# Kernel tuning notes

Hardware: AMD Instinct MI355X
Metric: run time of the kernel (lower is better)

Reference implementation:

```python
import jax, jax.numpy as jnp
import numpy as np

INPUT_DIM = 512
HIDDEN_DIM = 1024


def glorot_normal(key, shape):
    fan_in, fan_out = shape[0], shape[1]
    std = jnp.sqrt(2.0 / (fan_in + fan_out))
    return std * jax.random.normal(key, shape, dtype=jnp.float32)


def setup_inputs() -> dict:
    key = jax.random.key(0)
    k1, k2, k3 = jax.random.split(key, 3)
    b, t = 32, 1024
    H = HIDDEN_DIM + INPUT_DIM
    x_btd = jax.random.normal(k1, (b, t, INPUT_DIM), dtype=jnp.float32)
    input_paddings = jnp.zeros((b, t), dtype=jnp.float32)
    kernel = glorot_normal(k2, (H, 4 * HIDDEN_DIM))  # [H, 4h]
    bias = jnp.zeros((4 * HIDDEN_DIM,), dtype=jnp.float32)
    h_init = glorot_normal(k3, (1, HIDDEN_DIM))
    return {"x_btd": x_btd, "input_paddings": input_paddings,
            "kernel": kernel, "bias": bias, "h_init": h_init}


def lstm_step(carry, x_bd, kernel, bias):
    h_bh, c_bh = carry
    x_bH = jnp.concatenate([x_bd, h_bh], axis=-1)          # [b, d+h]
    gate_out = jnp.einsum('bH,Hh->bh', x_bH, kernel) + bias  # [b, 4h]
    f, i, o, g = jnp.split(gate_out, 4, axis=-1)
    c_new = jax.nn.sigmoid(f) * c_bh + jax.nn.sigmoid(i) * jnp.tanh(g)
    h_new = jax.nn.sigmoid(o) * jnp.tanh(c_new)
    return (h_new, c_new), h_new


def reference(x_btd, input_paddings, kernel, bias, h_init) -> jnp.ndarray:
    del input_paddings
    b = x_btd.shape[0]
    h0 = jnp.tile(h_init, (b, 1))                # [b, h]
    c0 = jnp.zeros((b, HIDDEN_DIM), dtype=x_btd.dtype)
    x_tbd = jnp.transpose(x_btd, (1, 0, 2))      # [t, b, d]

    def step(carry, x_bd):
        return lstm_step(carry, x_bd, kernel, bias)

    _, h_tbh = jax.lax.scan(step, (h0, c0), x_tbd)
    return jnp.transpose(h_tbh, (1, 0, 2))       # [b, t, h]
```

## Files before the change

### kernel.cpp

```cpp
#include <hip/hip_runtime.h>


#define T_STEPS 1024
#define BATCH   32
#define DIN     512
#define HID     1024
#define KTOT    1536
#define NBLK    128
#define WCOLS   32
#define WSTR    1544
#define REDSTR  33
#define REDW    (32*REDSTR)
#define NSLOT   8
#define FLAGSTR 16

#define LDS_W_BYTES   (WCOLS*WSTR*2)
#define LDS_RED_BYTES (NSLOT*REDW*4)
#define LDS_H_BYTES   (256*2)
#define LDS_TOTAL     (LDS_W_BYTES + LDS_RED_BYTES + LDS_H_BYTES)

typedef __attribute__((ext_vector_type(8))) short  short8;
typedef __attribute__((ext_vector_type(4))) float  floatx4;
typedef __attribute__((ext_vector_type(4))) unsigned short ushort4_;

__device__ __forceinline__ unsigned short f2bf(float f) {
    unsigned u = __builtin_bit_cast(unsigned, f);
    u += 0x7FFFu + ((u >> 16) & 1u);
    return (unsigned short)(u >> 16);
}
__device__ __forceinline__ float sigf(float x) { return 1.f / (1.f + __expf(-x)); }
__device__ __forceinline__ float tanh_fast(float x) {
    float e = __expf(2.f * x);
    return 1.f - 2.f / (e + 1.f);
}

__device__ __forceinline__ floatx4 coh_load16(const void* p) {
    floatx4 v;
    asm volatile("global_load_dwordx4 %0, %1, off sc1" : "=v"(v) : "v"(p));
    return v;
}
__device__ __forceinline__ int coh_load4(const void* p) {
    int v;
    asm volatile("global_load_dword %0, %1, off sc1\n\ts_waitcnt vmcnt(0)"
                 : "=v"(v) : "v"(p) : "memory");
    return v;
}
__device__ __forceinline__ void coh_store16(void* p, short8 v) {
    asm volatile("global_store_dwordx4 %0, %1, off sc1" :: "v"(p), "v"(v) : "memory");
}
__device__ __forceinline__ void coh_store4(void* p, int v) {
    asm volatile("global_store_dword %0, %1, off sc1" :: "v"(p), "v"(v) : "memory");
}
__device__ __forceinline__ void wait_vm0() {
    asm volatile("s_waitcnt vmcnt(0)" ::: "memory");
}

__global__ __launch_bounds__(256) void prep_wt(const float* __restrict__ kern,
                                               unsigned short* __restrict__ wt) {
    __shared__ unsigned short tile[64][72];
    const int c0 = (blockIdx.x & 63) * 64;
    const int k0 = (blockIdx.x >> 6) * 64;
    const int cl = threadIdx.x & 63;
    const int kg = threadIdx.x >> 6;
    #pragma unroll
    for (int i = 0; i < 16; ++i) {
        int kl = kg * 16 + i;
        tile[cl][kl] = f2bf(kern[(k0 + kl) * 4096 + c0 + cl]);
    }
    __syncthreads();
    #pragma unroll
    for (int i = 0; i < 16; ++i) {
        int cc = kg * 16 + i;
        wt[(size_t)(c0 + cc) * KTOT + k0 + cl] = tile[cc][cl];
    }
}

__global__ __launch_bounds__(256) void prep_x(const float* __restrict__ x,
                                              unsigned short* __restrict__ xT) {
    const int row = blockIdx.x * 2 + (threadIdx.x >> 7);
    const int l   = threadIdx.x & 127;
    const int b = row >> 10, t = row & 1023;
    float4 v = ((const float4*)(x + (size_t)row * DIN))[l];
    ushort4_ o;
    o.x = f2bf(v.x); o.y = f2bf(v.y); o.z = f2bf(v.z); o.w = f2bf(v.w);
    *(ushort4_*)(xT + ((size_t)t * BATCH + b) * DIN + l * 4) = o;
}

__global__ __launch_bounds__(256) void init_h(const float* __restrict__ h_init,
                                              unsigned short* __restrict__ hbuf,
                                              int* __restrict__ flags) {
    if (blockIdx.x == 32) {
        for (int i = threadIdx.x; i < NBLK * FLAGSTR; i += 256) flags[i] = 0;
        return;
    }
    const int p0 = blockIdx.x * 4;
    const int u = threadIdx.x & 7;
    #pragma unroll
    for (int j = 0; j < 4; ++j) {
        const int p = p0 + j;
        hbuf[p * 256 + threadIdx.x] = f2bf(h_init[p * 8 + u]);
    }
}

__global__ __launch_bounds__(512, 2) void lstm_persist(
    const unsigned short* __restrict__ wt,
    const unsigned short* __restrict__ xT,
    unsigned short* __restrict__ hbuf,
    int* __restrict__ flags,
    const float* __restrict__ bias,
    float* __restrict__ out)
{
    extern __shared__ char smem[];
    unsigned short* ldsW = (unsigned short*)smem;
    float* red = (float*)(smem + LDS_W_BYTES);
    unsigned short* hLDS = (unsigned short*)(smem + LDS_W_BYTES + LDS_RED_BYTES);

    const int bk   = blockIdx.x;
    const int tid  = threadIdx.x;
    const int wave = tid >> 6;
    const int lane = tid & 63;
    const int lrow = lane & 15;
    const int kq   = lane >> 4;
    const bool isG = wave < 4;
    const int  sl  = wave & 3;

    for (int cl = wave; cl < WCOLS; cl += 8) {
        const int gcol = (cl >> 3) * HID + bk * 8 + (cl & 7);
        const unsigned short* src = wt + (size_t)gcol * KTOT;
        unsigned short* dst = ldsW + cl * WSTR;
        for (int k = lane * 8; k < KTOT; k += 512)
            *(short8*)(dst + k) = *(const short8*)(src + k);
    }

    const int pb = tid >> 3;
    const int pu = tid & 7;
    float bias_r[4];
    float c_state = 0.f;
    if (tid < 256) {
        #pragma unroll
        for (int g = 0; g < 4; ++g) bias_r[g] = bias[g * HID + bk * 8 + pu];
    }

    const int* myflag = flags + (sl * 32 + (lane & 31)) * FLAGSTR;
    __syncthreads();

    {
        floatx4 zero = {0.f, 0.f, 0.f, 0.f};
        floatx4 acc[2][2];
        acc[0][0] = zero; acc[0][1] = zero; acc[1][0] = zero; acc[1][1] = zero;
        if (isG) {
            const unsigned short* xb = xT;
            #pragma unroll
            for (int i = 0; i < 4; ++i) {
                const int kl = sl * 128 + i * 32 + kq * 8;
                short8 a0 = *(const short8*)(xb + lrow * DIN + kl);
                short8 a1 = *(const short8*)(xb + (lrow + 16) * DIN + kl);
                short8 b0 = *(const short8*)(ldsW + lrow * WSTR + kl);
                short8 b1 = *(const short8*)(ldsW + (lrow + 16) * WSTR + kl);
                acc[0][0] = __builtin_amdgcn_mfma_f32_16x16x32_bf16(a0, b0, acc[0][0], 0, 0, 0);
                acc[0][1] = __builtin_amdgcn_mfma_f32_16x16x32_bf16(a0, b1, acc[0][1], 0, 0, 0);
                acc[1][0] = __builtin_amdgcn_mfma_f32_16x16x32_bf16(a1, b0, acc[1][0], 0, 0, 0);
                acc[1][1] = __builtin_amdgcn_mfma_f32_16x16x32_bf16(a1, b1, acc[1][1], 0, 0, 0);
            }
        } else {
            floatx4 ha[8][2];
            #pragma unroll
            for (int i = 0; i < 8; ++i) {
                const int p = sl * 32 + i * 4 + kq;
                ha[i][0] = coh_load16(hbuf + p * 256 + lrow * 8);
                ha[i][1] = coh_load16(hbuf + p * 256 + (lrow + 16) * 8);
            }
            wait_vm0();
            __builtin_amdgcn_sched_barrier(0);
            #pragma unroll
            for (int i = 0; i < 8; ++i) {
                const int kw = 512 + sl * 256 + i * 32 + kq * 8;
                short8 a0 = __builtin_bit_cast(short8, ha[i][0]);
                short8 a1 = __builtin_bit_cast(short8, ha[i][1]);
                short8 b0 = *(const short8*)(ldsW + lrow * WSTR + kw);
                short8 b1 = *(const short8*)(ldsW + (lrow + 16) * WSTR + kw);
                acc[0][0] = __builtin_amdgcn_mfma_f32_16x16x32_bf16(a0, b0, acc[0][0], 0, 0, 0);
                acc[0][1] = __builtin_amdgcn_mfma_f32_16x16x32_bf16(a0, b1, acc[0][1], 0, 0, 0);
                acc[1][0] = __builtin_amdgcn_mfma_f32_16x16x32_bf16(a1, b0, acc[1][0], 0, 0, 0);
                acc[1][1] = __builtin_amdgcn_mfma_f32_16x16x32_bf16(a1, b1, acc[1][1], 0, 0, 0);
            }
        }
        #pragma unroll
        for (int mt = 0; mt < 2; ++mt)
            #pragma unroll
            for (int nt = 0; nt < 2; ++nt)
                #pragma unroll
                for (int r = 0; r < 4; ++r)
                    red[wave * REDW + (mt * 16 + kq * 4 + r) * REDSTR + (nt * 16 + lrow)]
                        = acc[mt][nt][r];
    }

    for (int t = 0; t < T_STEPS; ++t) {
        __syncthreads();

        floatx4 xa[4][2];
        if (isG && t + 1 < T_STEPS) {
            const unsigned short* xb = xT + (size_t)(t + 1) * (BATCH * DIN);
            #pragma unroll
            for (int i = 0; i < 4; ++i) {
                const int kl = sl * 128 + i * 32 + kq * 8;
                xa[i][0] = *(const floatx4*)(xb + lrow * DIN + kl);
                xa[i][1] = *(const floatx4*)(xb + (lrow + 16) * DIN + kl);
            }
        }

        float gv[4];
        if (tid < 256) {
            #pragma unroll
            for (int g = 0; g < 4; ++g) {
                const int col = g * 8 + pu;
                float s = bias_r[g];
                #pragma unroll
                for (int w = 0; w < NSLOT; ++w) s += red[w * REDW + pb * REDSTR + col];
                gv[g] = s;
            }
            const float fg = sigf(gv[0]);
            const float ig = sigf(gv[1]);
            const float og = sigf(gv[2]);
            const float gg = tanh_fast(gv[3]);
            c_state = fg * c_state + ig * gg;
            const float hn = og * tanh_fast(c_state);
            out[(size_t)pb * (T_STEPS * HID) + (size_t)t * HID + bk * 8 + pu] = hn;
            hLDS[tid] = f2bf(hn);
        }
        if (t == T_STEPS - 1) break;

        __syncthreads();

        floatx4 zero = {0.f, 0.f, 0.f, 0.f};
        floatx4 acc[2][2];
        acc[0][0] = zero; acc[0][1] = zero; acc[1][0] = zero; acc[1][1] = zero;

        if (isG) {
            if (wave == 0) {
                if (lane < 32) {
                    short8 v = *(const short8*)(hLDS + lane * 8);
                    unsigned short* hp = hbuf + (size_t)((t + 1) & 1) * (NBLK * 256)
                                              + bk * 256 + lane * 8;
                    coh_store16(hp, v);
                }
                wait_vm0();
                if (lane == 0)
                    coh_store4(flags + bk * FLAGSTR, t + 1);
            }
            #pragma unroll
            for (int i = 0; i < 4; ++i) {
                const int kl = sl * 128 + i * 32 + kq * 8;
                short8 a0 = __builtin_bit_cast(short8, xa[i][0]);
                short8 a1 = __builtin_bit_cast(short8, xa[i][1]);
                short8 b0 = *(const short8*)(ldsW + lrow * WSTR + kl);
                short8 b1 = *(const short8*)(ldsW + (lrow + 16) * WSTR + kl);
                acc[0][0] = __builtin_amdgcn_mfma_f32_16x16x32_bf16(a0, b0, acc[0][0], 0, 0, 0);
                acc[0][1] = __builtin_amdgcn_mfma_f32_16x16x32_bf16(a0, b1, acc[0][1], 0, 0, 0);
                acc[1][0] = __builtin_amdgcn_mfma_f32_16x16x32_bf16(a1, b0, acc[1][0], 0, 0, 0);
                acc[1][1] = __builtin_amdgcn_mfma_f32_16x16x32_bf16(a1, b1, acc[1][1], 0, 0, 0);
            }
        } else {
            const int tgt = t + 1;
            while (coh_load4(myflag) < tgt)
                __builtin_amdgcn_s_sleep(1);
            const unsigned short* hb = hbuf + (size_t)((t + 1) & 1) * (NBLK * 256);
            floatx4 ha[8][2];
            #pragma unroll
            for (int i = 0; i < 8; ++i) {
                const int p = sl * 32 + i * 4 + kq;
                ha[i][0] = coh_load16(hb + p * 256 + lrow * 8);
                ha[i][1] = coh_load16(hb + p * 256 + (lrow + 16) * 8);
            }
            wait_vm0();
            __builtin_amdgcn_sched_barrier(0);
            #pragma unroll
            for (int i = 0; i < 8; ++i) {
                const int kw = 512 + sl * 256 + i * 32 + kq * 8;
                short8 a0 = __builtin_bit_cast(short8, ha[i][0]);
                short8 a1 = __builtin_bit_cast(short8, ha[i][1]);
                short8 b0 = *(const short8*)(ldsW + lrow * WSTR + kw);
                short8 b1 = *(const short8*)(ldsW + (lrow + 16) * WSTR + kw);
                acc[0][0] = __builtin_amdgcn_mfma_f32_16x16x32_bf16(a0, b0, acc[0][0], 0, 0, 0);
                acc[0][1] = __builtin_amdgcn_mfma_f32_16x16x32_bf16(a0, b1, acc[0][1], 0, 0, 0);
                acc[1][0] = __builtin_amdgcn_mfma_f32_16x16x32_bf16(a1, b0, acc[1][0], 0, 0, 0);
                acc[1][1] = __builtin_amdgcn_mfma_f32_16x16x32_bf16(a1, b1, acc[1][1], 0, 0, 0);
            }
        }

        #pragma unroll
        for (int mt = 0; mt < 2; ++mt)
            #pragma unroll
            for (int nt = 0; nt < 2; ++nt)
                #pragma unroll
                for (int r = 0; r < 4; ++r)
                    red[wave * REDW + (mt * 16 + kq * 4 + r) * REDSTR + (nt * 16 + lrow)]
                        = acc[mt][nt][r];
    }
}

extern "C" void kernel_launch(void* const* d_in, const int* in_sizes, int n_in,
                              void* d_out, int out_size, void* d_ws, size_t ws_size,
                              hipStream_t stream) {
    (void)in_sizes; (void)n_in; (void)out_size;
    const float* x      = (const float*)d_in[0];
    const float* kern   = (const float*)d_in[2];
    const float* bias   = (const float*)d_in[3];
    const float* h_init = (const float*)d_in[4];
    float* out = (float*)d_out;

    char* ws = (char*)d_ws;
    unsigned short* wt    = (unsigned short*)(ws);
    unsigned short* xT    = (unsigned short*)(ws + 12582912);
    unsigned short* hbuf  = (unsigned short*)(ws + 12582912 + 33554432);
    int*            flags = (int*)(ws + 12582912 + 33554432 + 131072);
    (void)ws_size;

    hipFuncSetAttribute((const void*)lstm_persist,
                        hipFuncAttributeMaxDynamicSharedMemorySize, LDS_TOTAL);

    prep_wt<<<dim3(64 * 24), dim3(256), 0, stream>>>(kern, wt);
    prep_x<<<dim3(BATCH * T_STEPS / 2), dim3(256), 0, stream>>>(x, xT);
    init_h<<<dim3(33), dim3(256), 0, stream>>>(h_init, hbuf, flags);

    void* args[] = { &wt, &xT, &hbuf, &flags, &bias, &out };
    hipLaunchCooperativeKernel((const void*)lstm_persist, dim3(NBLK), dim3(512),
                               args, LDS_TOTAL, stream);
}
```

Measured before the change: 4.356 ms.

## Keep weights in registers, double-buffer LDS atomic reduction, drop per-step barrier

Each wave now holds its slice of the bf16 weight matrix in VGPRs instead of staging all weights in LDS, which removes the LDS B-operand reads inside the MFMA loops. Partial gate sums are combined with LDS float atomic adds into a double-buffered reduction array that is pre-seeded with bias, and a single wave computes the gate nonlinearities for four outputs per lane at raised priority. That wave publishes h and its flag directly, which removes the second __syncthreads per timestep. The x prefetch now happens after the current step's MFMAs. The cost is much higher register pressure from the weight fragments, and LDS atomic contention across the eight waves.

```diff
diff --git a/kernel.cpp b/kernel.cpp
--- a/kernel.cpp
+++ b/kernel.cpp
@@ -7,21 +7,16 @@
 #define HID     1024
 #define KTOT    1536
 #define NBLK    128
-#define WCOLS   32
-#define WSTR    1544
 #define REDSTR  33
-#define REDW    (32*REDSTR)
-#define NSLOT   8
+#define REDCELLS (32*REDSTR)
 #define FLAGSTR 16
-
-#define LDS_W_BYTES   (WCOLS*WSTR*2)
-#define LDS_RED_BYTES (NSLOT*REDW*4)
-#define LDS_H_BYTES   (256*2)
-#define LDS_TOTAL     (LDS_W_BYTES + LDS_RED_BYTES + LDS_H_BYTES)
 
 typedef __attribute__((ext_vector_type(8))) short  short8;
 typedef __attribute__((ext_vector_type(4))) float  floatx4;
 typedef __attribute__((ext_vector_type(4))) unsigned short ushort4_;
+typedef __attribute__((ext_vector_type(2))) unsigned int   uint2_;
+
+#define MFMA16(a,b,c) __builtin_amdgcn_mfma_f32_16x16x32_bf16(a, b, c, 0, 0, 0)
 
 __device__ __forceinline__ unsigned short f2bf(float f) {
     unsigned u = __builtin_bit_cast(unsigned, f);
@@ -32,6 +27,9 @@
 __device__ __forceinline__ float tanh_fast(float x) {
     float e = __expf(2.f * x);
     return 1.f - 2.f / (e + 1.f);
+}
+__device__ __forceinline__ void lds_add(float* p, float v) {
+    __hip_atomic_fetch_add(p, v, __ATOMIC_RELAXED, __HIP_MEMORY_SCOPE_WORKGROUP);
 }
 
 __device__ __forceinline__ floatx4 coh_load16(const void* p) {
@@ -45,8 +43,8 @@
                  : "=v"(v) : "v"(p) : "memory");
     return v;
 }
-__device__ __forceinline__ void coh_store16(void* p, short8 v) {
-    asm volatile("global_store_dwordx4 %0, %1, off sc1" :: "v"(p), "v"(v) : "memory");
+__device__ __forceinline__ void coh_store8(void* p, uint2_ v) {
+    asm volatile("global_store_dwordx2 %0, %1, off sc1" :: "v"(p), "v"(v) : "memory");
 }
 __device__ __forceinline__ void coh_store4(void* p, int v) {
     asm volatile("global_store_dword %0, %1, off sc1" :: "v"(p), "v"(v) : "memory");
@@ -110,10 +108,7 @@
     const float* __restrict__ bias,
     float* __restrict__ out)
 {
-    extern __shared__ char smem[];
-    unsigned short* ldsW = (unsigned short*)smem;
-    float* red = (float*)(smem + LDS_W_BYTES);
-    unsigned short* hLDS = (unsigned short*)(smem + LDS_W_BYTES + LDS_RED_BYTES);
+    __shared__ float red[2][REDCELLS];
 
     const int bk   = blockIdx.x;
     const int tid  = threadIdx.x;
@@ -124,43 +119,65 @@
     const bool isG = wave < 4;
     const int  sl  = wave & 3;
 
-    for (int cl = wave; cl < WCOLS; cl += 8) {
-        const int gcol = (cl >> 3) * HID + bk * 8 + (cl & 7);
-        const unsigned short* src = wt + (size_t)gcol * KTOT;
-        unsigned short* dst = ldsW + cl * WSTR;
-        for (int k = lane * 8; k < KTOT; k += 512)
-            *(short8*)(dst + k) = *(const short8*)(src + k);
-    }
-
-    const int pb = tid >> 3;
-    const int pu = tid & 7;
-    float bias_r[4];
-    float c_state = 0.f;
-    if (tid < 256) {
-        #pragma unroll
-        for (int g = 0; g < 4; ++g) bias_r[g] = bias[g * HID + bk * 8 + pu];
-    }
-
+    short8 wb[8][2];
+    if (isG) {
+        #pragma unroll
+        for (int i = 0; i < 4; ++i) {
+            const int k = sl * 128 + i * 32 + kq * 8;
+            #pragma unroll
+            for (int c = 0; c < 2; ++c) {
+                const int cl = lrow + c * 16;
+                const int gcol = (cl >> 3) * HID + bk * 8 + (cl & 7);
+                wb[i][c] = *(const short8*)(wt + (size_t)gcol * KTOT + k);
+            }
+        }
+    } else {
+        #pragma unroll
+        for (int i = 0; i < 8; ++i) {
+            const int k = 512 + sl * 256 + i * 32 + kq * 8;
+            #pragma unroll
+            for (int c = 0; c < 2; ++c) {
+                const int cl = lrow + c * 16;
+                const int gcol = (cl >> 3) * HID + bk * 8 + (cl & 7);
+                wb[i][c] = *(const short8*)(wt + (size_t)gcol * KTOT + k);
+            }
+        }
+    }
+
+    const int pb = lane & 31;
+    const int ju = (lane >> 5) * 4;
+    float bias_r[4][4];
+    float c_st[4] = {0.f, 0.f, 0.f, 0.f};
+    if (wave == 0) {
+        #pragma unroll
+        for (int g = 0; g < 4; ++g)
+            #pragma unroll
+            for (int j = 0; j < 4; ++j)
+                bias_r[g][j] = bias[g * HID + bk * 8 + ju + j];
+    }
+
+    for (int idx = tid; idx < 2 * 1024; idx += 512) {
+        const int bsel = idx >> 10, cell = idx & 1023;
+        const int row = cell >> 5, col = cell & 31;
+        red[bsel][row * REDSTR + col] = bias[(col >> 3) * HID + bk * 8 + (col & 7)];
+    }
     const int* myflag = flags + (sl * 32 + (lane & 31)) * FLAGSTR;
     __syncthreads();
 
     {
-        floatx4 zero = {0.f, 0.f, 0.f, 0.f};
-        floatx4 acc[2][2];
-        acc[0][0] = zero; acc[0][1] = zero; acc[1][0] = zero; acc[1][1] = zero;
+        const floatx4 zero = {0.f, 0.f, 0.f, 0.f};
+        floatx4 acc[2][2] = {{zero, zero}, {zero, zero}};
         if (isG) {
             const unsigned short* xb = xT;
             #pragma unroll
             for (int i = 0; i < 4; ++i) {
-                const int kl = sl * 128 + i * 32 + kq * 8;
-                short8 a0 = *(const short8*)(xb + lrow * DIN + kl);
-                short8 a1 = *(const short8*)(xb + (lrow + 16) * DIN + kl);
-                short8 b0 = *(const short8*)(ldsW + lrow * WSTR + kl);
-                short8 b1 = *(const short8*)(ldsW + (lrow + 16) * WSTR + kl);
-                acc[0][0] = __builtin_amdgcn_mfma_f32_16x16x32_bf16(a0, b0, acc[0][0], 0, 0, 0);
-                acc[0][1] = __builtin_amdgcn_mfma_f32_16x16x32_bf16(a0, b1, acc[0][1], 0, 0, 0);
-                acc[1][0] = __builtin_amdgcn_mfma_f32_16x16x32_bf16(a1, b0, acc[1][0], 0, 0, 0);
-                acc[1][1] = __builtin_amdgcn_mfma_f32_16x16x32_bf16(a1, b1, acc[1][1], 0, 0, 0);
+                const int k = sl * 128 + i * 32 + kq * 8;
+                short8 a0 = *(const short8*)(xb + lrow * DIN + k);
+                short8 a1 = *(const short8*)(xb + (lrow + 16) * DIN + k);
+                acc[0][0] = MFMA16(a0, wb[i][0], acc[0][0]);
+                acc[0][1] = MFMA16(a0, wb[i][1], acc[0][1]);
+                acc[1][0] = MFMA16(a1, wb[i][0], acc[1][0]);
+                acc[1][1] = MFMA16(a1, wb[i][1], acc[1][1]);
             }
         } else {
             floatx4 ha[8][2];
@@ -174,15 +191,12 @@
             __builtin_amdgcn_sched_barrier(0);
             #pragma unroll
             for (int i = 0; i < 8; ++i) {
-                const int kw = 512 + sl * 256 + i * 32 + kq * 8;
                 short8 a0 = __builtin_bit_cast(short8, ha[i][0]);
                 short8 a1 = __builtin_bit_cast(short8, ha[i][1]);
-                short8 b0 = *(const short8*)(ldsW + lrow * WSTR + kw);
-                short8 b1 = *(const short8*)(ldsW + (lrow + 16) * WSTR + kw);
-                acc[0][0] = __builtin_amdgcn_mfma_f32_16x16x32_bf16(a0, b0, acc[0][0], 0, 0, 0);
-                acc[0][1] = __builtin_amdgcn_mfma_f32_16x16x32_bf16(a0, b1, acc[0][1], 0, 0, 0);
-                acc[1][0] = __builtin_amdgcn_mfma_f32_16x16x32_bf16(a1, b0, acc[1][0], 0, 0, 0);
-                acc[1][1] = __builtin_amdgcn_mfma_f32_16x16x32_bf16(a1, b1, acc[1][1], 0, 0, 0);
+                acc[0][0] = MFMA16(a0, wb[i][0], acc[0][0]);
+                acc[0][1] = MFMA16(a0, wb[i][1], acc[0][1]);
+                acc[1][0] = MFMA16(a1, wb[i][0], acc[1][0]);
+                acc[1][1] = MFMA16(a1, wb[i][1], acc[1][1]);
             }
         }
         #pragma unroll
@@ -191,74 +205,94 @@
             for (int nt = 0; nt < 2; ++nt)
                 #pragma unroll
                 for (int r = 0; r < 4; ++r)
-                    red[wave * REDW + (mt * 16 + kq * 4 + r) * REDSTR + (nt * 16 + lrow)]
-                        = acc[mt][nt][r];
+                    lds_add(&red[0][(mt * 16 + kq * 4 + r) * REDSTR + nt * 16 + lrow],
+                            acc[mt][nt][r]);
+    }
+
+    floatx4 xa[4][2];
+    if (isG) {
+        const unsigned short* xb = xT + (size_t)1 * (BATCH * DIN);
+        #pragma unroll
+        for (int i = 0; i < 4; ++i) {
+            const int k = sl * 128 + i * 32 + kq * 8;
+            xa[i][0] = *(const floatx4*)(xb + lrow * DIN + k);
+            xa[i][1] = *(const floatx4*)(xb + (lrow + 16) * DIN + k);
+        }
     }
 
     for (int t = 0; t < T_STEPS; ++t) {
         __syncthreads();
-
-        floatx4 xa[4][2];
-        if (isG && t + 1 < T_STEPS) {
-            const unsigned short* xb = xT + (size_t)(t + 1) * (BATCH * DIN);
+        float* rc = &red[t & 1][0];
+        float* rn = &red[(t + 1) & 1][0];
+
+        if (wave == 0) {
+            __builtin_amdgcn_s_setprio(1);
+            float rv[4][4];
+            #pragma unroll
+            for (int g = 0; g < 4; ++g)
+                #pragma unroll
+                for (int j = 0; j < 4; ++j)
+                    rv[g][j] = rc[pb * REDSTR + g * 8 + ju + j];
+            float hn[4];
+            #pragma unroll
+            for (int j = 0; j < 4; ++j) {
+                const float fg = sigf(rv[0][j]);
+                const float ig = sigf(rv[1][j]);
+                const float og = sigf(rv[2][j]);
+                const float gg = tanh_fast(rv[3][j]);
+                c_st[j] = fg * c_st[j] + ig * gg;
+                hn[j] = og * tanh_fast(c_st[j]);
+            }
+            if (t + 1 < T_STEPS) {
+                uint2_ hv;
+                hv.x = (unsigned)f2bf(hn[0]) | ((unsigned)f2bf(hn[1]) << 16);
+                hv.y = (unsigned)f2bf(hn[2]) | ((unsigned)f2bf(hn[3]) << 16);
+                coh_store8(hbuf + (size_t)((t + 1) & 1) * (NBLK * 256)
+                                + bk * 256 + pb * 8 + (lane >> 5) * 4, hv);
+                wait_vm0();
+                if (lane == 0) coh_store4(flags + bk * FLAGSTR, t + 1);
+            }
+            __builtin_amdgcn_s_setprio(0);
+            #pragma unroll
+            for (int g = 0; g < 4; ++g)
+                #pragma unroll
+                for (int j = 0; j < 4; ++j)
+                    rc[pb * REDSTR + g * 8 + ju + j] = bias_r[g][j];
+            floatx4 ov = {hn[0], hn[1], hn[2], hn[3]};
+            *(floatx4*)(out + (size_t)pb * (T_STEPS * HID) + (size_t)t * HID
+                        + bk * 8 + ju) = ov;
+        }
+
+        if (t + 1 >= T_STEPS) break;
+
+        const floatx4 zero = {0.f, 0.f, 0.f, 0.f};
+        floatx4 acc[2][2] = {{zero, zero}, {zero, zero}};
+        if (isG) {
             #pragma unroll
             for (int i = 0; i < 4; ++i) {
-                const int kl = sl * 128 + i * 32 + kq * 8;
-                xa[i][0] = *(const floatx4*)(xb + lrow * DIN + kl);
-                xa[i][1] = *(const floatx4*)(xb + (lrow + 16) * DIN + kl);
-            }
-        }
-
-        float gv[4];
-        if (tid < 256) {
-            #pragma unroll
-            for (int g = 0; g < 4; ++g) {
-                const int col = g * 8 + pu;
-                float s = bias_r[g];
-                #pragma unroll
-                for (int w = 0; w < NSLOT; ++w) s += red[w * REDW + pb * REDSTR + col];
-                gv[g] = s;
-            }
-            const float fg = sigf(gv[0]);
-            const float ig = sigf(gv[1]);
-            const float og = sigf(gv[2]);
-            const float gg = tanh_fast(gv[3]);
-            c_state = fg * c_state + ig * gg;
-            const float hn = og * tanh_fast(c_state);
-            out[(size_t)pb * (T_STEPS * HID) + (size_t)t * HID + bk * 8 + pu] = hn;
-            hLDS[tid] = f2bf(hn);
-        }
-        if (t == T_STEPS - 1) break;
-
-        __syncthreads();
-
-        floatx4 zero = {0.f, 0.f, 0.f, 0.f};
-        floatx4 acc[2][2];
-        acc[0][0] = zero; acc[0][1] = zero; acc[1][0] = zero; acc[1][1] = zero;
-
-        if (isG) {
-            if (wave == 0) {
-                if (lane < 32) {
-                    short8 v = *(const short8*)(hLDS + lane * 8);
-                    unsigned short* hp = hbuf + (size_t)((t + 1) & 1) * (NBLK * 256)
-                                              + bk * 256 + lane * 8;
-                    coh_store16(hp, v);
-                }
-                wait_vm0();
-                if (lane == 0)
-                    coh_store4(flags + bk * FLAGSTR, t + 1);
-            }
-            #pragma unroll
-            for (int i = 0; i < 4; ++i) {
-                const int kl = sl * 128 + i * 32 + kq * 8;
                 short8 a0 = __builtin_bit_cast(short8, xa[i][0]);
                 short8 a1 = __builtin_bit_cast(short8, xa[i][1]);
-                short8 b0 = *(const short8*)(ldsW + lrow * WSTR + kl);
-                short8 b1 = *(const short8*)(ldsW + (lrow + 16) * WSTR + kl);
-                acc[0][0] = __builtin_amdgcn_mfma_f32_16x16x32_bf16(a0, b0, acc[0][0], 0, 0, 0);
-                acc[0][1] = __builtin_amdgcn_mfma_f32_16x16x32_bf16(a0, b1, acc[0][1], 0, 0, 0);
-                acc[1][0] = __builtin_amdgcn_mfma_f32_16x16x32_bf16(a1, b0, acc[1][0], 0, 0, 0);
-                acc[1][1] = __builtin_amdgcn_mfma_f32_16x16x32_bf16(a1, b1, acc[1][1], 0, 0, 0);
+                acc[0][0] = MFMA16(a0, wb[i][0], acc[0][0]);
+                acc[0][1] = MFMA16(a0, wb[i][1], acc[0][1]);
+                acc[1][0] = MFMA16(a1, wb[i][0], acc[1][0]);
+                acc[1][1] = MFMA16(a1, wb[i][1], acc[1][1]);
+            }
+            #pragma unroll
+            for (int mt = 0; mt < 2; ++mt)
+                #pragma unroll
+                for (int nt = 0; nt < 2; ++nt)
+                    #pragma unroll
+                    for (int r = 0; r < 4; ++r)
+                        lds_add(&rn[(mt * 16 + kq * 4 + r) * REDSTR + nt * 16 + lrow],
+                                acc[mt][nt][r]);
+            if (t + 2 < T_STEPS) {
+                const unsigned short* xb = xT + (size_t)(t + 2) * (BATCH * DIN);
+                #pragma unroll
+                for (int i = 0; i < 4; ++i) {
+                    const int k = sl * 128 + i * 32 + kq * 8;
+                    xa[i][0] = *(const floatx4*)(xb + lrow * DIN + k);
+                    xa[i][1] = *(const floatx4*)(xb + (lrow + 16) * DIN + k);
+                }
             }
         } else {
             const int tgt = t + 1;
@@ -276,26 +310,22 @@
             __builtin_amdgcn_sched_barrier(0);
             #pragma unroll
             for (int i = 0; i < 8; ++i) {
-                const int kw = 512 + sl * 256 + i * 32 + kq * 8;
                 short8 a0 = __builtin_bit_cast(short8, ha[i][0]);
                 short8 a1 = __builtin_bit_cast(short8, ha[i][1]);
-                short8 b0 = *(const short8*)(ldsW + lrow * WSTR + kw);
-                short8 b1 = *(const short8*)(ldsW + (lrow + 16) * WSTR + kw);
-                acc[0][0] = __builtin_amdgcn_mfma_f32_16x16x32_bf16(a0, b0, acc[0][0], 0, 0, 0);
-                acc[0][1] = __builtin_amdgcn_mfma_f32_16x16x32_bf16(a0, b1, acc[0][1], 0, 0, 0);
-                acc[1][0] = __builtin_amdgcn_mfma_f32_16x16x32_bf16(a1, b0, acc[1][0], 0, 0, 0);
-                acc[1][1] = __builtin_amdgcn_mfma_f32_16x16x32_bf16(a1, b1, acc[1][1], 0, 0, 0);
-            }
-        }
-
-        #pragma unroll
-        for (int mt = 0; mt < 2; ++mt)
-            #pragma unroll
-            for (int nt = 0; nt < 2; ++nt)
-                #pragma unroll
-                for (int r = 0; r < 4; ++r)
-                    red[wave * REDW + (mt * 16 + kq * 4 + r) * REDSTR + (nt * 16 + lrow)]
-                        = acc[mt][nt][r];
+                acc[0][0] = MFMA16(a0, wb[i][0], acc[0][0]);
+                acc[0][1] = MFMA16(a0, wb[i][1], acc[0][1]);
+                acc[1][0] = MFMA16(a1, wb[i][0], acc[1][0]);
+                acc[1][1] = MFMA16(a1, wb[i][1], acc[1][1]);
+            }
+            #pragma unroll
+            for (int mt = 0; mt < 2; ++mt)
+                #pragma unroll
+                for (int nt = 0; nt < 2; ++nt)
+                    #pragma unroll
+                    for (int r = 0; r < 4; ++r)
+                        lds_add(&rn[(mt * 16 + kq * 4 + r) * REDSTR + nt * 16 + lrow],
+                                acc[mt][nt][r]);
+        }
     }
 }
 
@@ -316,14 +346,11 @@
     int*            flags = (int*)(ws + 12582912 + 33554432 + 131072);
     (void)ws_size;
 
-    hipFuncSetAttribute((const void*)lstm_persist,
-                        hipFuncAttributeMaxDynamicSharedMemorySize, LDS_TOTAL);
-
     prep_wt<<<dim3(64 * 24), dim3(256), 0, stream>>>(kern, wt);
     prep_x<<<dim3(BATCH * T_STEPS / 2), dim3(256), 0, stream>>>(x, xT);
     init_h<<<dim3(33), dim3(256), 0, stream>>>(h_init, hbuf, flags);
 
     void* args[] = { &wt, &xT, &hbuf, &flags, &bias, &out };
     hipLaunchCooperativeKernel((const void*)lstm_persist, dim3(NBLK), dim3(512),
-                               args, LDS_TOTAL, stream);
-}
+                               args, 0, stream);
+}
```

After: 10.83 ms. 2.49x slower.
